# Optimization experiments

Measured on AMD Instinct MI355X. Metric: run time of the kernel, lower is better.

The kernel has to match this reference:

```python
import jax, jax.numpy as jnp
import numpy as np

B, L, D = 4, 512, 768
NUM_SPANS = 4096
MAX_WIDTH = 8
DFF = 4 * D


def setup_inputs() -> dict:
    key = jax.random.key(0)
    k_h, k_s, k_w, k1, k2 = jax.random.split(key, 5)
    h = jax.random.normal(k_h, (B, L, D), dtype=jnp.float32)
    starts = jax.random.randint(k_s, (B, NUM_SPANS), 0, L)
    widths = jax.random.randint(k_w, (B, NUM_SPANS), 1, MAX_WIDTH + 1)
    ends = jnp.minimum(starts + widths - 1, L - 1)
    span_idx = jnp.stack([starts, ends], axis=-1).astype(jnp.int64 if jax.config.jax_enable_x64 else jnp.int32)
    W1 = jax.random.normal(k1, (D, DFF), dtype=jnp.float32) * (1.0 / np.sqrt(D))
    b1 = jnp.zeros((DFF,), dtype=jnp.float32)
    W2 = jax.random.normal(k2, (DFF, D), dtype=jnp.float32) * (1.0 / np.sqrt(DFF))
    b2 = jnp.zeros((D,), dtype=jnp.float32)
    return {"h": h, "span_idx": span_idx, "W1": W1, "b1": b1, "W2": W2, "b2": b2,
            "max_width": MAX_WIDTH}


def reference(h, span_idx, W1, b1, W2, b2, max_width):
    # h: [B, L, D]; span_idx: [B, S, 2] (start, end inclusive)
    Bv, Lv, Dv = h.shape
    starts = span_idx[:, :, 0]                       # [B, S]
    lengths = span_idx[:, :, 1] - starts + 1         # [B, S]
    offsets = jnp.arange(max_width)                  # static bound on span length
    positions = starts[:, :, None] + offsets[None, None, :]      # [B, S, W]
    mask = offsets[None, None, :] < lengths[:, :, None]          # [B, S, W]
    positions = jnp.clip(positions * mask, 0, Lv - 1)
    # indexed gather-reduce (no [B,S,L,D] broadcast): [B, S, W, D]
    gathered = h[jnp.arange(Bv)[:, None, None], positions]
    summed = jnp.sum(gathered * mask[..., None].astype(h.dtype), axis=2)  # [B, S, D]
    span_reps = summed / lengths[..., None].astype(h.dtype)
    # projection: Linear -> ReLU -> (Dropout: identity at eval) -> Linear
    hmid = jax.nn.relu(jnp.einsum('bsd,df->bsf', span_reps, W1) + b1)
    out = jnp.einsum('bsf,fd->bsd', hmid, W2) + b2
    return out
```

## Files before the change

### kernel.cpp

```cpp
#include <hip/hip_runtime.h>
#include <stdint.h>

#define B_DIM 4
#define L_DIM 512
#define D_DIM 768
#define S_DIM 4096
#define DFF_DIM 3072
#define M_DIM (B_DIM * S_DIM)

typedef unsigned short ushort_t;
typedef __attribute__((ext_vector_type(8))) short short8;
typedef __attribute__((ext_vector_type(4))) float floatx4;

__device__ __forceinline__ ushort_t f2bf(float x) {
  unsigned int u = __float_as_uint(x);
  u += 0x7FFFu + ((u >> 16) & 1u);
  return (ushort_t)(u >> 16);
}

__device__ __forceinline__ void load_lds16(const ushort_t* g, ushort_t* lds) {
  __builtin_amdgcn_global_load_lds(
      (const __attribute__((address_space(1))) unsigned int*)g,
      (__attribute__((address_space(3))) unsigned int*)lds, 16, 0, 0);
}

__device__ __forceinline__ void transpose_body(const float* __restrict__ in,
                                               ushort_t* __restrict__ out,
                                               int K, int N, int kb, int nb) {
  __shared__ float tile[32][33];
  const int k0 = kb * 32;
  const int n0 = nb * 32;
  const int tx = threadIdx.x & 31;
  const int ty = threadIdx.x >> 5;
#pragma unroll
  for (int r = 0; r < 32; r += 8)
    tile[ty + r][tx] = in[(long)(k0 + ty + r) * N + n0 + tx];
  __syncthreads();
#pragma unroll
  for (int r = 0; r < 32; r += 8)
    out[(long)(n0 + ty + r) * K + k0 + tx] = f2bf(tile[tx][ty + r]);
}

__device__ __forceinline__ void span_body(const float* __restrict__ h,
                                          const int* __restrict__ span_idx,
                                          ushort_t* __restrict__ A, int blk) {
  const int wave = threadIdx.x >> 6;
  const int lane = threadIdx.x & 63;
  const int span = blk * 4 + wave;
  const int b = span >> 12;
  const int start = span_idx[span * 2 + 0];
  const int end   = span_idx[span * 2 + 1];
  const float inv = 1.0f / (float)(end - start + 1);
  const float* hb = h + ((long)b * L_DIM + start) * D_DIM + lane;
  float a[12];
#pragma unroll
  for (int c = 0; c < 12; ++c) a[c] = 0.0f;
  for (int p = start; p <= end; ++p) {
#pragma unroll
    for (int c = 0; c < 12; ++c) a[c] += hb[c * 64];
    hb += D_DIM;
  }
  ushort_t* o = A + (long)span * D_DIM + lane;
#pragma unroll
  for (int c = 0; c < 12; ++c) o[c * 64] = f2bf(a[c] * inv);
}

__global__ __launch_bounds__(256)
void prep(const float* __restrict__ W1, ushort_t* __restrict__ W1T,
          const float* __restrict__ W2, ushort_t* __restrict__ W2T,
          const float* __restrict__ h, const int* __restrict__ span_idx,
          ushort_t* __restrict__ A) {
  const int blk = blockIdx.x;
  if (blk < 2304) {
    transpose_body(W1, W1T, D_DIM, DFF_DIM, blk % 24, blk / 24);
  } else if (blk < 4608) {
    const int b = blk - 2304;
    transpose_body(W2, W2T, DFF_DIM, D_DIM, b % 96, b / 96);
  } else {
    span_body(h, span_idx, A, blk - 4608);
  }
}

template <int MODE>
__global__ __launch_bounds__(256)
void gemm_bt(const ushort_t* __restrict__ A, const ushort_t* __restrict__ Bt,
             const float* __restrict__ bias, void* __restrict__ Cv,
             int M, int N, int K) {
  __shared__ ushort_t As[2][128 * 32];
  __shared__ ushort_t Bs[2][128 * 32];

  const int tid  = threadIdx.x;
  const int lane = tid & 63;
  const int wave = tid >> 6;
  const int l16  = lane & 15;
  const int quad = lane >> 4;

  const int bm = blockIdx.x;
  const int bn = blockIdx.y;

  const int wm = (wave & 1) * 64;
  const int wn = (wave >> 1) * 64;

  const int swz  = (l16 & 3) ^ ((l16 >> 2) & 3);
  const int coff = (quad ^ swz) * 8;

  floatx4 acc[4][4];
#pragma unroll
  for (int i = 0; i < 4; ++i)
#pragma unroll
    for (int j = 0; j < 4; ++j)
      acc[i][j] = (floatx4)0.0f;

  const int s0 = tid, s1 = tid + 256;
  const int r0 = s0 >> 2, r1 = s1 >> 2;
  const int c0 = (s0 & 3) ^ (r0 & 3) ^ ((r0 >> 2) & 3);
  const int c1 = (s1 & 3) ^ (r1 & 3) ^ ((r1 >> 2) & 3);
  const ushort_t* gA0 = A + (long)(bm * 128 + r0) * K + c0 * 8;
  const ushort_t* gA1 = A + (long)(bm * 128 + r1) * K + c1 * 8;
  const ushort_t* gB0 = Bt + (long)(bn * 128 + r0) * K + c0 * 8;
  const ushort_t* gB1 = Bt + (long)(bn * 128 + r1) * K + c1 * 8;

  const int nk = K >> 5;

  load_lds16(gA0, &As[0][0] + s0 * 8);
  load_lds16(gA1, &As[0][0] + s1 * 8);
  load_lds16(gB0, &Bs[0][0] + s0 * 8);
  load_lds16(gB1, &Bs[0][0] + s1 * 8);

  for (int k = 0; k < nk; ++k) {
    const int cur = k & 1;
    const int nxt = cur ^ 1;
    __syncthreads();

    if (k + 1 < nk) {
      const int off = (k + 1) * 32;
      load_lds16(gA0 + off, &As[nxt][0] + s0 * 8);
      load_lds16(gA1 + off, &As[nxt][0] + s1 * 8);
      load_lds16(gB0 + off, &Bs[nxt][0] + s0 * 8);
      load_lds16(gB1 + off, &Bs[nxt][0] + s1 * 8);
    }

    short8 af[4], bf[4];
#pragma unroll
    for (int i = 0; i < 4; ++i)
      af[i] = *(const short8*)(&As[cur][0] + (wm + i * 16 + l16) * 32 + coff);
#pragma unroll
    for (int j = 0; j < 4; ++j)
      bf[j] = *(const short8*)(&Bs[cur][0] + (wn + j * 16 + l16) * 32 + coff);
#pragma unroll
    for (int i = 0; i < 4; ++i)
#pragma unroll
      for (int j = 0; j < 4; ++j)
        acc[i][j] = __builtin_amdgcn_mfma_f32_16x16x32_bf16(af[i], bf[j], acc[i][j], 0, 0, 0);
  }

#pragma unroll
  for (int i = 0; i < 4; ++i) {
#pragma unroll
    for (int j = 0; j < 4; ++j) {
      const int col = bn * 128 + wn + j * 16 + l16;
      const float bv = bias[col];
      const int row0 = bm * 128 + wm + i * 16 + quad * 4;
#pragma unroll
      for (int r = 0; r < 4; ++r) {
        float v = acc[i][j][r] + bv;
        if (MODE == 0) {
          v = v > 0.0f ? v : 0.0f;
          ((ushort_t*)Cv)[(long)(row0 + r) * N + col] = f2bf(v);
        } else {
          ((float*)Cv)[(long)(row0 + r) * N + col] = v;
        }
      }
    }
  }
}

extern "C" void kernel_launch(void* const* d_in, const int* in_sizes, int n_in,
                              void* d_out, int out_size, void* d_ws, size_t ws_size,
                              hipStream_t stream) {
  const float* h        = (const float*)d_in[0];
  const int*   span_idx = (const int*)d_in[1];
  const float* W1       = (const float*)d_in[2];
  const float* b1       = (const float*)d_in[3];
  const float* W2       = (const float*)d_in[4];
  const float* b2       = (const float*)d_in[5];
  float* out = (float*)d_out;

  ushort_t* A   = (ushort_t*)d_ws;
  ushort_t* W1T = A + (size_t)M_DIM * D_DIM;
  ushort_t* W2T = W1T + (size_t)DFF_DIM * D_DIM;
  ushort_t* Hm  = W2T + (size_t)D_DIM * DFF_DIM;

  prep<<<2304 + 2304 + M_DIM / 4, 256, 0, stream>>>(W1, W1T, W2, W2T, h, span_idx, A);

  gemm_bt<0><<<dim3(M_DIM / 128, DFF_DIM / 128), 256, 0, stream>>>(
      A, W1T, b1, Hm, M_DIM, DFF_DIM, D_DIM);

  gemm_bt<1><<<dim3(M_DIM / 128, D_DIM / 128), 256, 0, stream>>>(
      Hm, W2T, b2, out, M_DIM, D_DIM, DFF_DIM);
}
```

Measured before the change: 279.4 us.

## Replace 128x128 GEMM with 256x256 tile, 8-wave pipelined MFMA kernel

Replaces the 128x128x32 tile GEMM (4 waves) with a 256x256x64 tile kernel of 8 waves. It stages the next K-tile in two halves, interleaved with four MFMA sub-phases that are separated by barriers and s_setprio. The larger tile raises arithmetic intensity and cuts global and LDS traffic per FLOP. The finer-grained schedule aims to overlap global-to-LDS loads with matrix math. The costs are 128 KB of LDS per block, many more barriers, and fewer blocks in the grid: 64x12 for GEMM1 and only 64x3=192 for GEMM2, which may underfill the CUs.

```diff
diff --git a/kernel.cpp b/kernel.cpp
--- a/kernel.cpp
+++ b/kernel.cpp
@@ -23,6 +23,13 @@
       (const __attribute__((address_space(1))) unsigned int*)g,
       (__attribute__((address_space(3))) unsigned int*)lds, 16, 0, 0);
 }
+
+#define BARRIER()                              \
+  do {                                         \
+    asm volatile("" ::: "memory");             \
+    __builtin_amdgcn_s_barrier();              \
+    asm volatile("" ::: "memory");             \
+  } while (0)
 
 __device__ __forceinline__ void transpose_body(const float* __restrict__ in,
                                                ushort_t* __restrict__ out,
@@ -82,93 +89,191 @@
 }
 
 template <int MODE>
-__global__ __launch_bounds__(256)
-void gemm_bt(const ushort_t* __restrict__ A, const ushort_t* __restrict__ Bt,
+__global__ __launch_bounds__(512, 2)
+void gemm256(const ushort_t* __restrict__ A, const ushort_t* __restrict__ Bt,
              const float* __restrict__ bias, void* __restrict__ Cv,
              int M, int N, int K) {
-  __shared__ ushort_t As[2][128 * 32];
-  __shared__ ushort_t Bs[2][128 * 32];
+  __shared__ ushort_t As[2][256 * 64];
+  __shared__ ushort_t Bs[2][256 * 64];
 
   const int tid  = threadIdx.x;
   const int lane = tid & 63;
-  const int wave = tid >> 6;
   const int l16  = lane & 15;
   const int quad = lane >> 4;
+  const int wave = tid >> 6;
+  const int wr   = wave >> 2;
+  const int wc   = wave & 3;
 
   const int bm = blockIdx.x;
   const int bn = blockIdx.y;
 
-  const int wm = (wave & 1) * 64;
-  const int wn = (wave >> 1) * 64;
-
-  const int swz  = (l16 & 3) ^ ((l16 >> 2) & 3);
-  const int coff = (quad ^ swz) * 8;
-
-  floatx4 acc[4][4];
-#pragma unroll
-  for (int i = 0; i < 4; ++i)
-#pragma unroll
-    for (int j = 0; j < 4; ++j)
-      acc[i][j] = (floatx4)0.0f;
-
-  const int s0 = tid, s1 = tid + 256;
-  const int r0 = s0 >> 2, r1 = s1 >> 2;
-  const int c0 = (s0 & 3) ^ (r0 & 3) ^ ((r0 >> 2) & 3);
-  const int c1 = (s1 & 3) ^ (r1 & 3) ^ ((r1 >> 2) & 3);
-  const ushort_t* gA0 = A + (long)(bm * 128 + r0) * K + c0 * 8;
-  const ushort_t* gA1 = A + (long)(bm * 128 + r1) * K + c1 * 8;
-  const ushort_t* gB0 = Bt + (long)(bn * 128 + r0) * K + c0 * 8;
-  const ushort_t* gB1 = Bt + (long)(bn * 128 + r1) * K + c1 * 8;
-
-  const int nk = K >> 5;
-
-  load_lds16(gA0, &As[0][0] + s0 * 8);
-  load_lds16(gA1, &As[0][0] + s1 * 8);
-  load_lds16(gB0, &Bs[0][0] + s0 * 8);
-  load_lds16(gB1, &Bs[0][0] + s1 * 8);
+  const int srow   = tid >> 3;
+  const int schunk = (tid & 7) ^ (srow & 7);
+  const ushort_t* gA = A  + (long)(bm * 256 + srow) * K + schunk * 8;
+  const ushort_t* gB = Bt + (long)(bn * 256 + srow) * K + schunk * 8;
+  const long rK64 = (long)K * 64;
+  ushort_t* lA = &As[0][0] + tid * 8;
+  ushort_t* lB = &Bs[0][0] + tid * 8;
+
+  auto STAGE_LO = [&](int buf, int kt) {
+    const ushort_t* ga = gA + (long)kt * 64;
+    const ushort_t* gb = gB + (long)kt * 64;
+    ushort_t* la = lA + buf * (256 * 64);
+    ushort_t* lb = lB + buf * (256 * 64);
+    load_lds16(ga,        la);
+    load_lds16(ga + rK64, la + 4096);
+    load_lds16(gb,        lb);
+    load_lds16(gb + rK64, lb + 4096);
+  };
+  auto STAGE_HI = [&](int buf, int kt) {
+    const ushort_t* ga = gA + (long)kt * 64 + 2 * rK64;
+    const ushort_t* gb = gB + (long)kt * 64 + 2 * rK64;
+    ushort_t* la = lA + buf * (256 * 64);
+    ushort_t* lb = lB + buf * (256 * 64);
+    load_lds16(ga,        la + 8192);
+    load_lds16(ga + rK64, la + 12288);
+    load_lds16(gb,        lb + 8192);
+    load_lds16(gb + rK64, lb + 12288);
+  };
+
+  const int arow0 = (wr * 128 + l16) * 64;
+  const int brow0 = (wc * 64 + l16) * 64;
+  const int cx0 = ((quad)     ^ (l16 & 7)) << 3;
+  const int cx1 = ((quad + 4) ^ (l16 & 7)) << 3;
+
+  floatx4 acc[8][4];
+#pragma unroll
+  for (int i = 0; i < 8; ++i)
+#pragma unroll
+    for (int j = 0; j < 4; ++j) acc[i][j] = (floatx4)0.0f;
+
+  const int nk = K >> 6;
+
+  STAGE_LO(0, 0);
+  STAGE_HI(0, 0);
+  if (nk > 1) {
+    STAGE_LO(1, 1);
+    asm volatile("s_waitcnt vmcnt(4)" ::: "memory");
+  } else {
+    asm volatile("s_waitcnt vmcnt(0)" ::: "memory");
+  }
+  BARRIER();
+
+  short8 af[4][2], bf[4][2];
 
   for (int k = 0; k < nk; ++k) {
     const int cur = k & 1;
     const int nxt = cur ^ 1;
-    __syncthreads();
-
-    if (k + 1 < nk) {
-      const int off = (k + 1) * 32;
-      load_lds16(gA0 + off, &As[nxt][0] + s0 * 8);
-      load_lds16(gA1 + off, &As[nxt][0] + s1 * 8);
-      load_lds16(gB0 + off, &Bs[nxt][0] + s0 * 8);
-      load_lds16(gB1 + off, &Bs[nxt][0] + s1 * 8);
-    }
-
-    short8 af[4], bf[4];
+    const ushort_t* Ac = &As[cur][0];
+    const ushort_t* Bc = &Bs[cur][0];
+
+    if (k + 1 < nk) STAGE_HI(nxt, k + 1);
+#pragma unroll
+    for (int i = 0; i < 4; ++i) {
+      af[i][0] = *(const short8*)(Ac + arow0 + i * 1024 + cx0);
+      af[i][1] = *(const short8*)(Ac + arow0 + i * 1024 + cx1);
+    }
+#pragma unroll
+    for (int j = 0; j < 2; ++j) {
+      bf[j][0] = *(const short8*)(Bc + brow0 + j * 1024 + cx0);
+      bf[j][1] = *(const short8*)(Bc + brow0 + j * 1024 + cx1);
+    }
+    BARRIER();
+    asm volatile("s_waitcnt lgkmcnt(0)" ::: "memory");
+    __builtin_amdgcn_sched_barrier(0);
+    __builtin_amdgcn_s_setprio(1);
 #pragma unroll
     for (int i = 0; i < 4; ++i)
-      af[i] = *(const short8*)(&As[cur][0] + (wm + i * 16 + l16) * 32 + coff);
-#pragma unroll
-    for (int j = 0; j < 4; ++j)
-      bf[j] = *(const short8*)(&Bs[cur][0] + (wn + j * 16 + l16) * 32 + coff);
+#pragma unroll
+      for (int j = 0; j < 2; ++j) {
+        acc[i][j] = __builtin_amdgcn_mfma_f32_16x16x32_bf16(af[i][0], bf[j][0], acc[i][j], 0, 0, 0);
+        acc[i][j] = __builtin_amdgcn_mfma_f32_16x16x32_bf16(af[i][1], bf[j][1], acc[i][j], 0, 0, 0);
+      }
+    __builtin_amdgcn_s_setprio(0);
+    BARRIER();
+
+#pragma unroll
+    for (int j = 0; j < 2; ++j) {
+      bf[2 + j][0] = *(const short8*)(Bc + brow0 + (2 + j) * 1024 + cx0);
+      bf[2 + j][1] = *(const short8*)(Bc + brow0 + (2 + j) * 1024 + cx1);
+    }
+    BARRIER();
+    asm volatile("s_waitcnt lgkmcnt(0)" ::: "memory");
+    __builtin_amdgcn_sched_barrier(0);
+    __builtin_amdgcn_s_setprio(1);
 #pragma unroll
     for (int i = 0; i < 4; ++i)
 #pragma unroll
-      for (int j = 0; j < 4; ++j)
-        acc[i][j] = __builtin_amdgcn_mfma_f32_16x16x32_bf16(af[i], bf[j], acc[i][j], 0, 0, 0);
-  }
-
-#pragma unroll
-  for (int i = 0; i < 4; ++i) {
-#pragma unroll
-    for (int j = 0; j < 4; ++j) {
-      const int col = bn * 128 + wn + j * 16 + l16;
-      const float bv = bias[col];
-      const int row0 = bm * 128 + wm + i * 16 + quad * 4;
+      for (int j = 0; j < 2; ++j) {
+        acc[i][2 + j] = __builtin_amdgcn_mfma_f32_16x16x32_bf16(af[i][0], bf[2 + j][0], acc[i][2 + j], 0, 0, 0);
+        acc[i][2 + j] = __builtin_amdgcn_mfma_f32_16x16x32_bf16(af[i][1], bf[2 + j][1], acc[i][2 + j], 0, 0, 0);
+      }
+    __builtin_amdgcn_s_setprio(0);
+    BARRIER();
+
+#pragma unroll
+    for (int i = 0; i < 4; ++i) {
+      af[i][0] = *(const short8*)(Ac + arow0 + (4 + i) * 1024 + cx0);
+      af[i][1] = *(const short8*)(Ac + arow0 + (4 + i) * 1024 + cx1);
+    }
+    BARRIER();
+    asm volatile("s_waitcnt lgkmcnt(0)" ::: "memory");
+    __builtin_amdgcn_sched_barrier(0);
+    __builtin_amdgcn_s_setprio(1);
+#pragma unroll
+    for (int i = 0; i < 4; ++i)
+#pragma unroll
+      for (int j = 0; j < 2; ++j) {
+        acc[4 + i][2 + j] = __builtin_amdgcn_mfma_f32_16x16x32_bf16(af[i][0], bf[2 + j][0], acc[4 + i][2 + j], 0, 0, 0);
+        acc[4 + i][2 + j] = __builtin_amdgcn_mfma_f32_16x16x32_bf16(af[i][1], bf[2 + j][1], acc[4 + i][2 + j], 0, 0, 0);
+      }
+    __builtin_amdgcn_s_setprio(0);
+    BARRIER();
+
+    if (k + 2 < nk) {
+      STAGE_LO(cur, k + 2);
+      __builtin_amdgcn_s_setprio(1);
+#pragma unroll
+      for (int i = 0; i < 4; ++i)
+#pragma unroll
+        for (int j = 0; j < 2; ++j) {
+          acc[4 + i][j] = __builtin_amdgcn_mfma_f32_16x16x32_bf16(af[i][0], bf[j][0], acc[4 + i][j], 0, 0, 0);
+          acc[4 + i][j] = __builtin_amdgcn_mfma_f32_16x16x32_bf16(af[i][1], bf[j][1], acc[4 + i][j], 0, 0, 0);
+        }
+      __builtin_amdgcn_s_setprio(0);
+      asm volatile("s_waitcnt vmcnt(4)" ::: "memory");
+    } else {
+      __builtin_amdgcn_s_setprio(1);
+#pragma unroll
+      for (int i = 0; i < 4; ++i)
+#pragma unroll
+        for (int j = 0; j < 2; ++j) {
+          acc[4 + i][j] = __builtin_amdgcn_mfma_f32_16x16x32_bf16(af[i][0], bf[j][0], acc[4 + i][j], 0, 0, 0);
+          acc[4 + i][j] = __builtin_amdgcn_mfma_f32_16x16x32_bf16(af[i][1], bf[j][1], acc[4 + i][j], 0, 0, 0);
+        }
+      __builtin_amdgcn_s_setprio(0);
+      asm volatile("s_waitcnt vmcnt(0)" ::: "memory");
+    }
+    BARRIER();
+  }
+
+  const long rowbase = (long)bm * 256 + wr * 128 + quad * 4;
+  const int  colbase = bn * 256 + wc * 64 + l16;
+#pragma unroll
+  for (int j = 0; j < 4; ++j) {
+    const int col = colbase + j * 16;
+    const float bv = bias[col];
+#pragma unroll
+    for (int i = 0; i < 8; ++i) {
+      const long row0 = rowbase + i * 16;
 #pragma unroll
       for (int r = 0; r < 4; ++r) {
         float v = acc[i][j][r] + bv;
         if (MODE == 0) {
           v = v > 0.0f ? v : 0.0f;
-          ((ushort_t*)Cv)[(long)(row0 + r) * N + col] = f2bf(v);
+          ((ushort_t*)Cv)[(row0 + r) * N + col] = f2bf(v);
         } else {
-          ((float*)Cv)[(long)(row0 + r) * N + col] = v;
+          ((float*)Cv)[(row0 + r) * N + col] = v;
         }
       }
     }
@@ -193,9 +298,9 @@
 
   prep<<<2304 + 2304 + M_DIM / 4, 256, 0, stream>>>(W1, W1T, W2, W2T, h, span_idx, A);
 
-  gemm_bt<0><<<dim3(M_DIM / 128, DFF_DIM / 128), 256, 0, stream>>>(
+  gemm256<0><<<dim3(M_DIM / 256, DFF_DIM / 256), 512, 0, stream>>>(
       A, W1T, b1, Hm, M_DIM, DFF_DIM, D_DIM);
 
-  gemm_bt<1><<<dim3(M_DIM / 128, D_DIM / 128), 256, 0, stream>>>(
+  gemm256<1><<<dim3(M_DIM / 256, D_DIM / 256), 512, 0, stream>>>(
       Hm, W2T, b2, out, M_DIM, D_DIM, DFF_DIM);
 }
```

Result: slower. 309.9 us (+10.9%).

## Keep full-K W1 slab resident in LDS for first GEMM and vectorize span pooling

Applied to the files above, without the earlier changes.

Replaces the first GEMM with a kernel that loads a full 96x768 bf16 slab of W1T into LDS once (swizzled) and streams A fragments directly from global memory into registers with software double-buffering. This removes the per-K-step syncthreads and LDS staging of A. Blocks are remapped so that tiles sharing B land on the same XCD. The span pooling now uses float4 loads and 4-wide bf16 stores. The trade-off is large LDS use (about 144KB per block), which limits occupancy, and uncached direct global reads of A.

```diff
diff --git a/kernel.cpp b/kernel.cpp
--- a/kernel.cpp
+++ b/kernel.cpp
@@ -10,6 +10,7 @@
 
 typedef unsigned short ushort_t;
 typedef __attribute__((ext_vector_type(8))) short short8;
+typedef __attribute__((ext_vector_type(4))) short short4v;
 typedef __attribute__((ext_vector_type(4))) float floatx4;
 
 __device__ __forceinline__ ushort_t f2bf(float x) {
@@ -51,18 +52,24 @@
   const int start = span_idx[span * 2 + 0];
   const int end   = span_idx[span * 2 + 1];
   const float inv = 1.0f / (float)(end - start + 1);
-  const float* hb = h + ((long)b * L_DIM + start) * D_DIM + lane;
-  float a[12];
-#pragma unroll
-  for (int c = 0; c < 12; ++c) a[c] = 0.0f;
+  const floatx4* hb =
+      (const floatx4*)(h + ((long)b * L_DIM + start) * D_DIM) + lane;
+  floatx4 a[3];
+#pragma unroll
+  for (int c = 0; c < 3; ++c) a[c] = (floatx4)0.0f;
   for (int p = start; p <= end; ++p) {
 #pragma unroll
-    for (int c = 0; c < 12; ++c) a[c] += hb[c * 64];
-    hb += D_DIM;
-  }
-  ushort_t* o = A + (long)span * D_DIM + lane;
-#pragma unroll
-  for (int c = 0; c < 12; ++c) o[c * 64] = f2bf(a[c] * inv);
+    for (int c = 0; c < 3; ++c) a[c] += hb[c * 64];
+    hb += 192;
+  }
+  short4v* o = (short4v*)(A + (long)span * D_DIM) + lane;
+#pragma unroll
+  for (int c = 0; c < 3; ++c) {
+    short4v s;
+#pragma unroll
+    for (int e = 0; e < 4; ++e) s[e] = (short)f2bf(a[c][e] * inv);
+    o[c * 64] = s;
+  }
 }
 
 __global__ __launch_bounds__(256)
@@ -81,6 +88,104 @@
   }
 }
 
+__global__ __launch_bounds__(512, 2)
+void gemm1_bres(const ushort_t* __restrict__ A, const ushort_t* __restrict__ Bt,
+                const float* __restrict__ bias, ushort_t* __restrict__ C) {
+  __shared__ ushort_t Bs[96 * 768];
+
+  const int tid  = threadIdx.x;
+  const int lane = tid & 63;
+  const int l16  = lane & 15;
+  const int quad = lane >> 4;
+  const int wave = tid >> 6;
+  const int wr   = wave >> 1;
+  const int wc   = wave & 1;
+
+  const int id  = blockIdx.x;
+  const int xcd = id & 7;
+  const int loc = id >> 3;
+  const int bm  = xcd * 8 + (loc & 7);
+  const int bn  = loc >> 3;
+
+  {
+    const ushort_t* src = Bt + (long)bn * 96 * 768;
+#pragma unroll
+    for (int i = 0; i < 18; ++i) {
+      const int s = tid + i * 512;
+      const int row = s / 96;
+      const int chunk = s - row * 96;
+      const int gchunk = chunk ^ (row & 7);
+      load_lds16(src + (long)row * 768 + gchunk * 8, &Bs[0] + s * 8);
+    }
+  }
+
+  const ushort_t* gA =
+      A + (long)(bm * 256 + wr * 64 + l16) * 768 + quad * 8;
+  const int t0 = wc * 48 + l16;
+
+  floatx4 acc[4][3];
+#pragma unroll
+  for (int m = 0; m < 4; ++m)
+#pragma unroll
+    for (int j = 0; j < 3; ++j) acc[m][j] = (floatx4)0.0f;
+
+  __syncthreads();
+
+  short8 aA[4], aB[4], bA[3], bB[3];
+#pragma unroll
+  for (int m = 0; m < 4; ++m)
+    aA[m] = *(const short8*)(gA + (long)m * (16 * 768));
+#pragma unroll
+  for (int j = 0; j < 3; ++j) {
+    const int t = t0 + j * 16;
+    bA[j] = *(const short8*)(&Bs[0] + (long)t * 768 + ((quad) ^ (t & 7)) * 8);
+  }
+
+#pragma unroll
+  for (int k = 0; k < 24; ++k) {
+    if (k + 1 < 24) {
+      const long ko = (long)(k + 1) * 32;
+#pragma unroll
+      for (int m = 0; m < 4; ++m)
+        aB[m] = *(const short8*)(gA + (long)m * (16 * 768) + ko);
+#pragma unroll
+      for (int j = 0; j < 3; ++j) {
+        const int t = t0 + j * 16;
+        bB[j] = *(const short8*)(&Bs[0] + (long)t * 768 +
+                                 (((k + 1) * 4 + quad) ^ (t & 7)) * 8);
+      }
+    }
+#pragma unroll
+    for (int m = 0; m < 4; ++m)
+#pragma unroll
+      for (int j = 0; j < 3; ++j)
+        acc[m][j] = __builtin_amdgcn_mfma_f32_16x16x32_bf16(aA[m], bA[j],
+                                                            acc[m][j], 0, 0, 0);
+#pragma unroll
+    for (int m = 0; m < 4; ++m) aA[m] = aB[m];
+#pragma unroll
+    for (int j = 0; j < 3; ++j) bA[j] = bB[j];
+  }
+
+  const long rowbase = (long)bm * 256 + wr * 64 + quad * 4;
+  const int  colbase = bn * 96 + wc * 48 + l16;
+#pragma unroll
+  for (int j = 0; j < 3; ++j) {
+    const int col = colbase + j * 16;
+    const float bv = bias[col];
+#pragma unroll
+    for (int m = 0; m < 4; ++m) {
+      const long row0 = rowbase + m * 16;
+#pragma unroll
+      for (int r = 0; r < 4; ++r) {
+        float v = acc[m][j][r] + bv;
+        v = v > 0.0f ? v : 0.0f;
+        C[(row0 + r) * DFF_DIM + col] = f2bf(v);
+      }
+    }
+  }
+}
+
 template <int MODE>
 __global__ __launch_bounds__(256)
 void gemm_bt(const ushort_t* __restrict__ A, const ushort_t* __restrict__ Bt,
@@ -193,8 +298,7 @@
 
   prep<<<2304 + 2304 + M_DIM / 4, 256, 0, stream>>>(W1, W1T, W2, W2T, h, span_idx, A);
 
-  gemm_bt<0><<<dim3(M_DIM / 128, DFF_DIM / 128), 256, 0, stream>>>(
-      A, W1T, b1, Hm, M_DIM, DFF_DIM, D_DIM);
+  gemm1_bres<<<dim3(2048), 512, 0, stream>>>(A, W1T, b1, Hm);
 
   gemm_bt<1><<<dim3(M_DIM / 128, D_DIM / 128), 256, 0, stream>>>(
       Hm, W2T, b2, out, M_DIM, D_DIM, DFF_DIM);
```

New measurement: 385.3 us. 1.38x slower.
